# Kernel optimization log

Measured on AMD Instinct MI355X. Metric: run time of the kernel, lower is better.

## Reference

```python
import jax, jax.numpy as jnp
import numpy as np
import math

NUM_HEADS = 8
LN_EPS = 1e-5
SINK_EPS = 1.0  # entropic eps in SinkhornDistance (eps=1)


def _layer_norm(x, g, b):
    m = jnp.mean(x, axis=-1, keepdims=True)
    v = jnp.var(x, axis=-1, keepdims=True)
    return (x - m) * jax.lax.rsqrt(v + LN_EPS) * g + b


def setup_inputs() -> dict:
    key = jax.random.key(0)
    ks = jax.random.split(key, 8)
    B, n, dQ, dV = 8, 1024, 512, 512
    s = 1.0 / math.sqrt(dV)
    return {
        "Q": jax.random.normal(ks[0], (B, n, dQ), jnp.float32),
        "K": jax.random.normal(ks[1], (B, n, dQ), jnp.float32),
        "Wq": jax.random.normal(ks[2], (dV, dQ), jnp.float32) * s,
        "bq": jax.random.normal(ks[3], (dV,), jnp.float32) * 0.01,
        "Wo": jax.random.normal(ks[4], (dV, dV), jnp.float32) * s,
        "bo": jax.random.normal(ks[5], (dV,), jnp.float32) * 0.01,
        "g0": jnp.ones((dV,), jnp.float32),
        "b0": jnp.zeros((dV,), jnp.float32),
        "g1": jnp.ones((dV,), jnp.float32),
        "b1": jnp.zeros((dV,), jnp.float32),
    }


def reference(Q, K, Wq, bq, Wo, bo, g0, b0, g1, b1):
    # K is accepted by the original forward but unused (K_ = V_ = Q_).
    B, n, _ = Q.shape
    dim_V = Wq.shape[0]
    H = NUM_HEADS
    d = dim_V // H

    Qp = Q @ Wq.T + bq                                   # [B, n, dim_V]
    # torch.cat(Q.split(d, 2), 0): head-major stacking -> [H*B, n, d]
    Q_ = Qp.reshape(B, n, H, d).transpose(2, 0, 1, 3).reshape(H * B, n, d)

    sqrtV = math.sqrt(math.sqrt(dim_V))
    X = Q_ / sqrtV
    # cost = dotmat(X, X) = -X X^T  (overall scaled by 1/sqrt(dim_V))
    C = -jnp.einsum('bnd,bmd->bnm', X, X)                # [HB, n, n]

    # log-domain Sinkhorn, eps=1, max_iter=1, mu = nu = 1/n
    log_mu = jnp.log(1.0 / n + 1e-8).astype(Q.dtype)
    M0 = -C / SINK_EPS
    u = SINK_EPS * (log_mu - jax.scipy.special.logsumexp(M0, axis=-1))         # [HB, n]
    v = SINK_EPS * (log_mu - jax.scipy.special.logsumexp(
        (-C + u[:, :, None]) / SINK_EPS, axis=1))                               # [HB, n]
    pi = jnp.exp((-C + u[:, :, None] + v[:, None, :]) / SINK_EPS)               # [HB, n, n]

    A = pi * n
    O_ = Q_ + jnp.einsum('bnm,bmd->bnd', A, Q_)          # [HB, n, d]
    # inverse head stacking -> [B, n, dim_V]
    O = O_.reshape(H, B, n, d).transpose(1, 2, 0, 3).reshape(B, n, dim_V)

    O = _layer_norm(O, g0, b0)
    O = O + jax.nn.relu(O @ Wo.T + bo)
    O = _layer_norm(O, g1, b1)
    return O
```

## Files before the change

kernel.cpp:

```cpp
#include <hip/hip_runtime.h>
#include <hip/hip_bf16.h>

typedef __bf16 bf16;
typedef __bf16 bf16x4 __attribute__((ext_vector_type(4)));
typedef __bf16 bf16x8 __attribute__((ext_vector_type(8)));
typedef float  f32x4  __attribute__((ext_vector_type(4)));

#define DEVI static __device__ __forceinline__

constexpr float SCALE_S = 0.04419417382415922f;
constexpr float LOG_MU  = -6.93146156565f;
constexpr int   LDT     = 72;

DEVI f32x4 mfma16(bf16x8 a, bf16x8 b, f32x4 c) {
    return __builtin_amdgcn_mfma_f32_16x16x32_bf16(a, b, c, 0, 0, 0);
}

DEVI bf16x8 cvt8(const float* __restrict__ p) {
    const float4 f0 = *(const float4*)p;
    const float4 f1 = *(const float4*)(p + 4);
    bf16x8 h;
    h[0] = (bf16)f0.x; h[1] = (bf16)f0.y; h[2] = (bf16)f0.z; h[3] = (bf16)f0.w;
    h[4] = (bf16)f1.x; h[5] = (bf16)f1.y; h[6] = (bf16)f1.z; h[7] = (bf16)f1.w;
    return h;
}

template<int EPI>
__global__ __launch_bounds__(256)
void gemm_kernel(const void* __restrict__ Ap, const float* __restrict__ Bm,
                 const float* __restrict__ bias, const bf16* __restrict__ X0,
                 bf16* __restrict__ outQh, bf16* __restrict__ outQhT,
                 float* __restrict__ outT)
{
    __shared__ bf16 sA[64 * LDT];
    __shared__ bf16 sB[64 * LDT];
    const int tid = threadIdx.x;
    const int rowBase = blockIdx.y * 64;
    const int colBase = blockIdx.x * 64;
    const int w = tid >> 6, lane = tid & 63, quad = lane >> 4, l16 = lane & 15;
    const int wr = (w >> 1) * 32, wc = (w & 1) * 32;

    f32x4 acc[2][2];
    #pragma unroll
    for (int i = 0; i < 2; ++i)
        #pragma unroll
        for (int j = 0; j < 2; ++j)
            #pragma unroll
            for (int e = 0; e < 4; ++e) acc[i][j][e] = 0.f;

    for (int kt = 0; kt < 512; kt += 64) {
        if (kt) __syncthreads();
        #pragma unroll
        for (int it = 0; it < 2; ++it) {
            int idx = it * 256 + tid;
            int r = idx >> 3, kb = idx & 7;
            if (EPI == 0) {
                *(bf16x8*)(&sA[r * LDT + kb * 8]) =
                    cvt8((const float*)Ap + (size_t)(rowBase + r) * 512 + kt + kb * 8);
            } else {
                *(uint4*)(&sA[r * LDT + kb * 8]) =
                    *(const uint4*)((const bf16*)Ap + (size_t)(rowBase + r) * 512 + kt + kb * 8);
            }
            *(bf16x8*)(&sB[r * LDT + kb * 8]) =
                cvt8(Bm + (size_t)(colBase + r) * 512 + kt + kb * 8);
        }
        __syncthreads();
        #pragma unroll
        for (int kk = 0; kk < 2; ++kk) {
            bf16x8 a[2], b[2];
            #pragma unroll
            for (int i = 0; i < 2; ++i)
                a[i] = *(const bf16x8*)(&sA[(wr + i * 16 + l16) * LDT + kk * 32 + quad * 8]);
            #pragma unroll
            for (int j = 0; j < 2; ++j)
                b[j] = *(const bf16x8*)(&sB[(wc + j * 16 + l16) * LDT + kk * 32 + quad * 8]);
            #pragma unroll
            for (int i = 0; i < 2; ++i)
                #pragma unroll
                for (int j = 0; j < 2; ++j)
                    acc[i][j] = mfma16(a[i], b[j], acc[i][j]);
        }
    }

    #pragma unroll
    for (int i = 0; i < 2; ++i) {
        #pragma unroll
        for (int j = 0; j < 2; ++j) {
            const int col = colBase + wc + j * 16 + l16;
            const float bv = bias[col];
            if (EPI == 0) {
                const int hh = col >> 6, jj = col & 63;
                const int rowA = rowBase + wr + i * 16 + quad * 4;
                const int bb = rowA >> 10, iib = rowA & 1023;
                const int bhh = (hh << 3) + bb;
                bf16x4 pk;
                #pragma unroll
                for (int rg = 0; rg < 4; ++rg) {
                    const float z = acc[i][j][rg] + bv;
                    pk[rg] = (bf16)z;
                    outQh[((size_t)(bhh * 1024 + iib + rg) << 6) + jj] = (bf16)z;
                }
                if (outQhT)
                    *(bf16x4*)(&outQhT[(((size_t)bhh * 64 + jj) << 10) + iib]) = pk;
            } else {
                #pragma unroll
                for (int rg = 0; rg < 4; ++rg) {
                    const int row = rowBase + wr + i * 16 + quad * 4 + rg;
                    const float z = acc[i][j][rg] + bv;
                    const float x0 = (float)X0[(size_t)row * 512 + col];
                    outT[(size_t)row * 512 + col] = x0 + fmaxf(z, 0.f);
                }
            }
        }
    }
}

template<int ADD_U>
__global__ __launch_bounds__(256, 4)
void sink_lse_kernel(const bf16* __restrict__ Qh, const float* __restrict__ uin,
                     float* __restrict__ out)
{
    __shared__ bf16 sQi[128 * LDT];
    __shared__ bf16 sQm[2][64 * LDT];
    __shared__ float su[1024];
    const int tid = threadIdx.x;
    const int bh = blockIdx.y;
    const int rowTile = blockIdx.x * 128;
    const bf16* Qb = Qh + ((size_t)bh << 16);

    #pragma unroll
    for (int it = 0; it < 4; ++it) {
        int idx = it * 256 + tid;
        int r = idx >> 3, kb = idx & 7;
        *(uint4*)(&sQi[r * LDT + kb * 8]) =
            *(const uint4*)(Qb + ((rowTile + r) << 6) + kb * 8);
    }
    if (ADD_U)
        *(float4*)(&su[tid * 4]) = *(const float4*)(uin + (bh << 10) + tid * 4);

    const int r0 = tid >> 3, kb0 = tid & 7;
    #pragma unroll
    for (int it = 0; it < 2; ++it)
        *(uint4*)(&sQm[0][(it * 32 + r0) * LDT + kb0 * 8]) =
            *(const uint4*)(Qb + ((it * 32 + r0) << 6) + kb0 * 8);
    __syncthreads();

    const int w = tid >> 6, lane = tid & 63, quad = lane >> 4, l16 = lane & 15;
    float rsum[2][4] = {{0.f,0.f,0.f,0.f},{0.f,0.f,0.f,0.f}};

    for (int mt = 0; mt < 16; ++mt) {
        const int cur = mt & 1;
        uint4 pf[2];
        if (mt < 15) {
            #pragma unroll
            for (int it = 0; it < 2; ++it)
                pf[it] = *(const uint4*)(Qb + (((mt + 1) * 64 + it * 32 + r0) << 6) + kb0 * 8);
        }

        f32x4 acc[2][4];
        #pragma unroll
        for (int a = 0; a < 2; ++a)
            #pragma unroll
            for (int ct = 0; ct < 4; ++ct)
                #pragma unroll
                for (int e = 0; e < 4; ++e) acc[a][ct][e] = 0.f;

        #pragma unroll
        for (int kk = 0; kk < 2; ++kk) {
            bf16x8 afr[2], bfr[4];
            #pragma unroll
            for (int a = 0; a < 2; ++a)
                afr[a] = *(const bf16x8*)(&sQi[(w * 32 + a * 16 + l16) * LDT + kk * 32 + quad * 8]);
            #pragma unroll
            for (int ct = 0; ct < 4; ++ct)
                bfr[ct] = *(const bf16x8*)(&sQm[cur][(ct * 16 + l16) * LDT + kk * 32 + quad * 8]);
            #pragma unroll
            for (int a = 0; a < 2; ++a)
                #pragma unroll
                for (int ct = 0; ct < 4; ++ct)
                    acc[a][ct] = mfma16(afr[a], bfr[ct], acc[a][ct]);
        }
        #pragma unroll
        for (int a = 0; a < 2; ++a)
            #pragma unroll
            for (int ct = 0; ct < 4; ++ct) {
                const float uadd = ADD_U ? su[mt * 64 + ct * 16 + l16] : 0.f;
                #pragma unroll
                for (int rg = 0; rg < 4; ++rg)
                    rsum[a][rg] += __expf(acc[a][ct][rg] * SCALE_S + uadd);
            }

        if (mt < 15) {
            #pragma unroll
            for (int it = 0; it < 2; ++it)
                *(uint4*)(&sQm[cur ^ 1][(it * 32 + r0) * LDT + kb0 * 8]) = pf[it];
        }
        __syncthreads();
    }
    #pragma unroll
    for (int off = 1; off < 16; off <<= 1)
        #pragma unroll
        for (int a = 0; a < 2; ++a)
            #pragma unroll
            for (int rg = 0; rg < 4; ++rg)
                rsum[a][rg] += __shfl_xor(rsum[a][rg], off);

    if (l16 == 0) {
        #pragma unroll
        for (int a = 0; a < 2; ++a)
            #pragma unroll
            for (int rg = 0; rg < 4; ++rg)
                out[(bh << 10) + rowTile + w * 32 + a * 16 + quad * 4 + rg] =
                    LOG_MU - __logf(rsum[a][rg]);
    }
}

template<int USE_T>
__global__ __launch_bounds__(256, 2)
void sink_av_kernel(const bf16* __restrict__ Qh, const bf16* __restrict__ QhT,
                    const float* __restrict__ u, const float* __restrict__ v,
                    float* __restrict__ O)
{
    __shared__ bf16 sQi[128 * LDT];
    __shared__ bf16 sQm[2][64 * LDT];
    __shared__ bf16 sQmT[2][64 * LDT];
    __shared__ bf16 sP[4][32 * LDT];
    __shared__ float sv[1024];
    const int tid = threadIdx.x;
    const int bh = blockIdx.y;
    const int rowTile = blockIdx.x * 128;
    const bf16* Qb = Qh + ((size_t)bh << 16);
    const bf16* QbT = QhT + ((size_t)bh << 16);
    const int w = tid >> 6, lane = tid & 63, quad = lane >> 4, l16 = lane & 15;
    const int r0 = tid >> 3, kb0 = tid & 7;

    #pragma unroll
    for (int it = 0; it < 4; ++it) {
        int idx = it * 256 + tid;
        int r = idx >> 3, kb = idx & 7;
        *(uint4*)(&sQi[r * LDT + kb * 8]) =
            *(const uint4*)(Qb + ((rowTile + r) << 6) + kb * 8);
    }
    *(float4*)(&sv[tid * 4]) = *(const float4*)(v + (bh << 10) + tid * 4);
    float u_r[2][4];
    #pragma unroll
    for (int a = 0; a < 2; ++a)
        #pragma unroll
        for (int rg = 0; rg < 4; ++rg)
            u_r[a][rg] = u[(bh << 10) + rowTile + w * 32 + a * 16 + quad * 4 + rg];

    #pragma unroll
    for (int it = 0; it < 2; ++it) {
        const int r = it * 32 + r0;
        uint4 val = *(const uint4*)(Qb + (r << 6) + kb0 * 8);
        *(uint4*)(&sQm[0][r * LDT + kb0 * 8]) = val;
        if (USE_T) {
            *(uint4*)(&sQmT[0][r * LDT + kb0 * 8]) =
                *(const uint4*)(QbT + (r << 10) + kb0 * 8);
        } else {
            union { uint4 q; bf16 e[8]; } cv; cv.q = val;
            #pragma unroll
            for (int j = 0; j < 8; ++j)
                sQmT[0][(kb0 * 8 + j) * LDT + r] = cv.e[j];
        }
    }
    __syncthreads();

    f32x4 accO[2][4];
    #pragma unroll
    for (int a = 0; a < 2; ++a)
        #pragma unroll
        for (int ct = 0; ct < 4; ++ct)
            #pragma unroll
            for (int e = 0; e < 4; ++e) accO[a][ct][e] = 0.f;

    for (int mt = 0; mt < 16; ++mt) {
        const int cur = mt & 1;
        uint4 pfm[2], pft[2];
        if (mt < 15) {
            #pragma unroll
            for (int it = 0; it < 2; ++it) {
                const int r = it * 32 + r0;
                pfm[it] = *(const uint4*)(Qb + (((mt + 1) * 64 + r) << 6) + kb0 * 8);
                if (USE_T)
                    pft[it] = *(const uint4*)(QbT + (r << 10) + (mt + 1) * 64 + kb0 * 8);
            }
        }

        f32x4 acc[2][4];
        #pragma unroll
        for (int a = 0; a < 2; ++a)
            #pragma unroll
            for (int ct = 0; ct < 4; ++ct)
                #pragma unroll
                for (int e = 0; e < 4; ++e) acc[a][ct][e] = 0.f;

        #pragma unroll
        for (int kk = 0; kk < 2; ++kk) {
            bf16x8 afr[2], bfr[4];
            #pragma unroll
            for (int a = 0; a < 2; ++a)
                afr[a] = *(const bf16x8*)(&sQi[(w * 32 + a * 16 + l16) * LDT + kk * 32 + quad * 8]);
            #pragma unroll
            for (int ct = 0; ct < 4; ++ct)
                bfr[ct] = *(const bf16x8*)(&sQm[cur][(ct * 16 + l16) * LDT + kk * 32 + quad * 8]);
            #pragma unroll
            for (int a = 0; a < 2; ++a)
                #pragma unroll
                for (int ct = 0; ct < 4; ++ct)
                    acc[a][ct] = mfma16(afr[a], bfr[ct], acc[a][ct]);
        }
        #pragma unroll
        for (int a = 0; a < 2; ++a)
            #pragma unroll
            for (int ct = 0; ct < 4; ++ct) {
                const float vv = sv[mt * 64 + ct * 16 + l16];
                #pragma unroll
                for (int rg = 0; rg < 4; ++rg) {
                    const float p = 1024.f * __expf(acc[a][ct][rg] * SCALE_S + u_r[a][rg] + vv);
                    sP[w][(a * 16 + quad * 4 + rg) * LDT + ct * 16 + l16] = (bf16)p;
                }
            }
        #pragma unroll
        for (int kk = 0; kk < 2; ++kk) {
            bf16x8 a2[2], b2[4];
            #pragma unroll
            for (int a = 0; a < 2; ++a)
                a2[a] = *(const bf16x8*)(&sP[w][(a * 16 + l16) * LDT + kk * 32 + quad * 8]);
            #pragma unroll
            for (int ct = 0; ct < 4; ++ct)
                b2[ct] = *(const bf16x8*)(&sQmT[cur][(ct * 16 + l16) * LDT + kk * 32 + quad * 8]);
            #pragma unroll
            for (int a = 0; a < 2; ++a)
                #pragma unroll
                for (int ct = 0; ct < 4; ++ct)
                    accO[a][ct] = mfma16(a2[a], b2[ct], accO[a][ct]);
        }

        if (mt < 15) {
            #pragma unroll
            for (int it = 0; it < 2; ++it) {
                const int r = it * 32 + r0;
                *(uint4*)(&sQm[cur ^ 1][r * LDT + kb0 * 8]) = pfm[it];
                if (USE_T) {
                    *(uint4*)(&sQmT[cur ^ 1][r * LDT + kb0 * 8]) = pft[it];
                } else {
                    union { uint4 q; bf16 e[8]; } cv; cv.q = pfm[it];
                    #pragma unroll
                    for (int j = 0; j < 8; ++j)
                        sQmT[cur ^ 1][(kb0 * 8 + j) * LDT + r] = cv.e[j];
                }
            }
        }
        __syncthreads();
    }

    const int hh = bh >> 3, bb = bh & 7;
    #pragma unroll
    for (int a = 0; a < 2; ++a)
        #pragma unroll
        for (int ct = 0; ct < 4; ++ct) {
            const int dcol = ct * 16 + l16;
            #pragma unroll
            for (int rg = 0; rg < 4; ++rg) {
                const int irow = w * 32 + a * 16 + quad * 4 + rg;
                const float o = (float)sQi[irow * LDT + dcol] + accO[a][ct][rg];
                O[((size_t)(bb * 1024 + rowTile + irow) << 9) + (hh << 6) + dcol] = o;
            }
        }
}

template<typename OutT>
__global__ __launch_bounds__(256)
void ln_kernel(const float* __restrict__ X, const float* __restrict__ g,
               const float* __restrict__ bb, OutT* __restrict__ out)
{
    const int row = blockIdx.x;
    const float* x = X + (size_t)row * 512;
    const float2 v2 = ((const float2*)x)[threadIdx.x];
    float s  = v2.x + v2.y;
    float ss = v2.x * v2.x + v2.y * v2.y;
    #pragma unroll
    for (int off = 32; off; off >>= 1) {
        s  += __shfl_down(s, off);
        ss += __shfl_down(ss, off);
    }
    __shared__ float red[8];
    const int w = threadIdx.x >> 6, lane = threadIdx.x & 63;
    if (lane == 0) { red[w] = s; red[4 + w] = ss; }
    __syncthreads();
    s  = red[0] + red[1] + red[2] + red[3];
    ss = red[4] + red[5] + red[6] + red[7];
    const float mean = s * (1.f / 512.f);
    const float var  = ss * (1.f / 512.f) - mean * mean;
    const float rstd = rsqrtf(var + 1e-5f);
    const int c = threadIdx.x * 2;
    const float y0 = (v2.x - mean) * rstd * g[c]     + bb[c];
    const float y1 = (v2.y - mean) * rstd * g[c + 1] + bb[c + 1];
    out[(size_t)row * 512 + c]     = (OutT)y0;
    out[(size_t)row * 512 + c + 1] = (OutT)y1;
}

extern "C" void kernel_launch(void* const* d_in, const int* in_sizes, int n_in,
                              void* d_out, int out_size, void* d_ws, size_t ws_size,
                              hipStream_t stream)
{
    const float* Q  = (const float*)d_in[0];
    const float* Wq = (const float*)d_in[2];
    const float* bq = (const float*)d_in[3];
    const float* Wo = (const float*)d_in[4];
    const float* bo = (const float*)d_in[5];
    const float* g0 = (const float*)d_in[6];
    const float* b0 = (const float*)d_in[7];
    const float* g1 = (const float*)d_in[8];
    const float* b1 = (const float*)d_in[9];

    char* ws = (char*)d_ws;
    const bool useT = ws_size >= (size_t)34078720;

    bf16 *Qh, *QhT, *X0;
    float *u, *v, *Obuf;
    if (useT) {
        Qh   = (bf16*)ws;
        QhT  = (bf16*)(ws + 8388608);
        X0   = (bf16*)(ws + 8388608);
        u    = (float*)(ws + 16777216);
        v    = (float*)(ws + 17039360);
        Obuf = (float*)(ws + 17301504);
    } else {
        Qh   = (bf16*)ws;
        QhT  = nullptr;
        X0   = (bf16*)ws;
        u    = (float*)(ws + 8388608);
        v    = (float*)(ws + 8650752);
        Obuf = (float*)(ws + 8912896);
    }

    gemm_kernel<0><<<dim3(8, 128), 256, 0, stream>>>(Q, Wq, bq, nullptr, Qh, QhT, nullptr);
    sink_lse_kernel<0><<<dim3(8, 64), 256, 0, stream>>>(Qh, nullptr, u);
    sink_lse_kernel<1><<<dim3(8, 64), 256, 0, stream>>>(Qh, u, v);
    if (useT)
        sink_av_kernel<1><<<dim3(8, 64), 256, 0, stream>>>(Qh, QhT, u, v, Obuf);
    else
        sink_av_kernel<0><<<dim3(8, 64), 256, 0, stream>>>(Qh, Qh, u, v, Obuf);
    ln_kernel<bf16><<<8192, 256, 0, stream>>>(Obuf, g0, b0, X0);
    gemm_kernel<1><<<dim3(8, 128), 256, 0, stream>>>(X0, Wo, bo, X0, nullptr, nullptr, Obuf);
    ln_kernel<float><<<8192, 256, 0, stream>>>(Obuf, g1, b1, (float*)d_out);
}
```

Baseline: 228.3 us.

## Pre-convert Q to bf16 and enlarge GEMM tiles to 128x64

Adds a separate kernel that converts Q to bf16 in workspace, so the projection GEMM loads bf16 A tiles directly instead of converting fp32 inline. Both GEMMs now use 128x64 block tiles, with each wave covering 32 rows by all 64 columns, which halves the grid and reuses B fragments more. The workspace fallback path is removed and the transposed-Q path is assumed always available. This adds an extra launch plus an extra read and write of Q, and it requires a larger workspace, roughly 59.8 MB.

Result: slower. 236.6 us (+3.7%).

```diff
diff --git a/kernel.cpp b/kernel.cpp
--- a/kernel.cpp
+++ b/kernel.cpp
@@ -25,59 +25,65 @@
     return h;
 }
 
+__global__ __launch_bounds__(256)
+void cvt_kernel(const float* __restrict__ in, bf16* __restrict__ out)
+{
+    const size_t i = ((size_t)blockIdx.x * 256 + threadIdx.x) * 8;
+    *(bf16x8*)(out + i) = cvt8(in + i);
+}
+
 template<int EPI>
 __global__ __launch_bounds__(256)
-void gemm_kernel(const void* __restrict__ Ap, const float* __restrict__ Bm,
+void gemm_kernel(const bf16* __restrict__ A, const float* __restrict__ Bm,
                  const float* __restrict__ bias, const bf16* __restrict__ X0,
                  bf16* __restrict__ outQh, bf16* __restrict__ outQhT,
                  float* __restrict__ outT)
 {
-    __shared__ bf16 sA[64 * LDT];
+    __shared__ bf16 sA[128 * LDT];
     __shared__ bf16 sB[64 * LDT];
     const int tid = threadIdx.x;
-    const int rowBase = blockIdx.y * 64;
+    const int rowBase = blockIdx.y * 128;
     const int colBase = blockIdx.x * 64;
     const int w = tid >> 6, lane = tid & 63, quad = lane >> 4, l16 = lane & 15;
-    const int wr = (w >> 1) * 32, wc = (w & 1) * 32;
-
-    f32x4 acc[2][2];
+
+    f32x4 acc[2][4];
     #pragma unroll
     for (int i = 0; i < 2; ++i)
         #pragma unroll
-        for (int j = 0; j < 2; ++j)
+        for (int j = 0; j < 4; ++j)
             #pragma unroll
             for (int e = 0; e < 4; ++e) acc[i][j][e] = 0.f;
 
     for (int kt = 0; kt < 512; kt += 64) {
         if (kt) __syncthreads();
+        #pragma unroll
+        for (int it = 0; it < 4; ++it) {
+            int idx = it * 256 + tid;
+            int r = idx >> 3, kb = idx & 7;
+            *(uint4*)(&sA[r * LDT + kb * 8]) =
+                *(const uint4*)(A + (size_t)(rowBase + r) * 512 + kt + kb * 8);
+        }
         #pragma unroll
         for (int it = 0; it < 2; ++it) {
             int idx = it * 256 + tid;
             int r = idx >> 3, kb = idx & 7;
-            if (EPI == 0) {
-                *(bf16x8*)(&sA[r * LDT + kb * 8]) =
-                    cvt8((const float*)Ap + (size_t)(rowBase + r) * 512 + kt + kb * 8);
-            } else {
-                *(uint4*)(&sA[r * LDT + kb * 8]) =
-                    *(const uint4*)((const bf16*)Ap + (size_t)(rowBase + r) * 512 + kt + kb * 8);
-            }
             *(bf16x8*)(&sB[r * LDT + kb * 8]) =
                 cvt8(Bm + (size_t)(colBase + r) * 512 + kt + kb * 8);
         }
         __syncthreads();
         #pragma unroll
         for (int kk = 0; kk < 2; ++kk) {
-            bf16x8 a[2], b[2];
+            bf16x8 a[2], b[4];
             #pragma unroll
             for (int i = 0; i < 2; ++i)
-                a[i] = *(const bf16x8*)(&sA[(wr + i * 16 + l16) * LDT + kk * 32 + quad * 8]);
-            #pragma unroll
-            for (int j = 0; j < 2; ++j)
-                b[j] = *(const bf16x8*)(&sB[(wc + j * 16 + l16) * LDT + kk * 32 + quad * 8]);
+                a[i] = *(const bf16x8*)(&sA[(w * 32 + i * 16 + l16) * LDT + kk * 32 + quad * 8]);
+            #pragma unroll
+            for (int j = 0; j < 4; ++j)
+                b[j] = *(const bf16x8*)(&sB[(j * 16 + l16) * LDT + kk * 32 + quad * 8]);
             #pragma unroll
             for (int i = 0; i < 2; ++i)
                 #pragma unroll
-                for (int j = 0; j < 2; ++j)
+                for (int j = 0; j < 4; ++j)
                     acc[i][j] = mfma16(a[i], b[j], acc[i][j]);
         }
     }
@@ -85,12 +91,12 @@
     #pragma unroll
     for (int i = 0; i < 2; ++i) {
         #pragma unroll
-        for (int j = 0; j < 2; ++j) {
-            const int col = colBase + wc + j * 16 + l16;
+        for (int j = 0; j < 4; ++j) {
+            const int col = colBase + j * 16 + l16;
             const float bv = bias[col];
             if (EPI == 0) {
                 const int hh = col >> 6, jj = col & 63;
-                const int rowA = rowBase + wr + i * 16 + quad * 4;
+                const int rowA = rowBase + w * 32 + i * 16 + quad * 4;
                 const int bb = rowA >> 10, iib = rowA & 1023;
                 const int bhh = (hh << 3) + bb;
                 bf16x4 pk;
@@ -100,12 +106,11 @@
                     pk[rg] = (bf16)z;
                     outQh[((size_t)(bhh * 1024 + iib + rg) << 6) + jj] = (bf16)z;
                 }
-                if (outQhT)
-                    *(bf16x4*)(&outQhT[(((size_t)bhh * 64 + jj) << 10) + iib]) = pk;
+                *(bf16x4*)(&outQhT[(((size_t)bhh * 64 + jj) << 10) + iib]) = pk;
             } else {
                 #pragma unroll
                 for (int rg = 0; rg < 4; ++rg) {
-                    const int row = rowBase + wr + i * 16 + quad * 4 + rg;
+                    const int row = rowBase + w * 32 + i * 16 + quad * 4 + rg;
                     const float z = acc[i][j][rg] + bv;
                     const float x0 = (float)X0[(size_t)row * 512 + col];
                     outT[(size_t)row * 512 + col] = x0 + fmaxf(z, 0.f);
@@ -416,34 +421,20 @@
     const float* b1 = (const float*)d_in[9];
 
     char* ws = (char*)d_ws;
-    const bool useT = ws_size >= (size_t)34078720;
-
-    bf16 *Qh, *QhT, *X0;
-    float *u, *v, *Obuf;
-    if (useT) {
-        Qh   = (bf16*)ws;
-        QhT  = (bf16*)(ws + 8388608);
-        X0   = (bf16*)(ws + 8388608);
-        u    = (float*)(ws + 16777216);
-        v    = (float*)(ws + 17039360);
-        Obuf = (float*)(ws + 17301504);
-    } else {
-        Qh   = (bf16*)ws;
-        QhT  = nullptr;
-        X0   = (bf16*)ws;
-        u    = (float*)(ws + 8388608);
-        v    = (float*)(ws + 8650752);
-        Obuf = (float*)(ws + 8912896);
-    }
-
-    gemm_kernel<0><<<dim3(8, 128), 256, 0, stream>>>(Q, Wq, bq, nullptr, Qh, QhT, nullptr);
+    bf16*  Qh   = (bf16*)ws;
+    bf16*  QhT  = (bf16*)(ws + 8388608);
+    bf16*  X0   = (bf16*)(ws + 8388608);
+    float* u    = (float*)(ws + 16777216);
+    float* v    = (float*)(ws + 17039360);
+    float* Obuf = (float*)(ws + 17301504);
+    bf16*  Qbf  = (bf16*)(ws + 51380224);
+
+    cvt_kernel<<<2048, 256, 0, stream>>>(Q, Qbf);
+    gemm_kernel<0><<<dim3(8, 64), 256, 0, stream>>>(Qbf, Wq, bq, nullptr, Qh, QhT, nullptr);
     sink_lse_kernel<0><<<dim3(8, 64), 256, 0, stream>>>(Qh, nullptr, u);
     sink_lse_kernel<1><<<dim3(8, 64), 256, 0, stream>>>(Qh, u, v);
-    if (useT)
-        sink_av_kernel<1><<<dim3(8, 64), 256, 0, stream>>>(Qh, QhT, u, v, Obuf);
-    else
-        sink_av_kernel<0><<<dim3(8, 64), 256, 0, stream>>>(Qh, Qh, u, v, Obuf);
+    sink_av_kernel<1><<<dim3(8, 64), 256, 0, stream>>>(Qh, QhT, u, v, Obuf);
     ln_kernel<bf16><<<8192, 256, 0, stream>>>(Obuf, g0, b0, X0);
-    gemm_kernel<1><<<dim3(8, 128), 256, 0, stream>>>(X0, Wo, bo, X0, nullptr, nullptr, Obuf);
+    gemm_kernel<1><<<dim3(8, 64), 256, 0, stream>>>(X0, Wo, bo, X0, nullptr, nullptr, Obuf);
     ln_kernel<float><<<8192, 256, 0, stream>>>(Obuf, g1, b1, (float*)d_out);
 }
```
